# Optimization experiments

Hardware: AMD Instinct MI355X
Metric: run time of the kernel (lower is better)

Reference implementation:

```python
import jax, jax.numpy as jnp
import numpy as np

N_NODES = 50000
N_EDGES = 200000
NODE_DIM = 160     # node feat dim (divisible by 5 per wrapper slicing)
EDGE_DIM = 64      # latent edge feat dim
RAW_EDGE_DIM = 8   # raw geometric edge attributes
HID = 256          # hidden dim of edge/node update MLPs
ENC_HID = 128      # hidden dim of EASP edge encoder
N_ITER = 3
ENC_IN = 2 * NODE_DIM + RAW_EDGE_DIM                 # 328
EDGE_IN = 2 * 2 * NODE_DIM + 2 * EDGE_DIM            # 768 (reattach -> factor 2)
MSG_IN = 2 * NODE_DIM + EDGE_DIM                     # 384 (reattach node + edge)


def _ln(x, g, b):
    mu = jnp.mean(x, axis=-1, keepdims=True)
    v = jnp.var(x, axis=-1, keepdims=True)
    return (x - mu) * jax.lax.rsqrt(v + 1e-5) * g + b


def setup_inputs() -> dict:
    key = jax.random.key(0)
    ks = jax.random.split(key, 24)

    def w(k, shape):
        return (jax.random.normal(k, shape, jnp.float32) / np.sqrt(shape[0])).astype(jnp.float32)

    return {
        'x': jax.random.normal(ks[0], (N_NODES, NODE_DIM), jnp.float32),
        'edge_attr': jax.random.normal(ks[1], (N_EDGES, RAW_EDGE_DIM), jnp.float32),
        # EASP edge encoder MLP
        'enc_W1': w(ks[2], (ENC_IN, ENC_HID)), 'enc_b1': jnp.zeros((ENC_HID,), jnp.float32),
        'enc_W2': w(ks[3], (ENC_HID, EDGE_DIM)), 'enc_b2': jnp.zeros((EDGE_DIM,), jnp.float32),
        # EdgeCNN edge update MLP
        'eW1': w(ks[4], (EDGE_IN, HID)), 'eb1': jnp.zeros((HID,), jnp.float32),
        'eW2': w(ks[5], (HID, EDGE_DIM)), 'eb2': jnp.zeros((EDGE_DIM,), jnp.float32),
        # AttentionNodeUpdateNet: per-edge message MLP + attention vector + node out
        'mW1': w(ks[6], (MSG_IN, HID)), 'mb1': jnp.zeros((HID,), jnp.float32),
        'att_v': w(ks[7], (HID,)),
        'nW1': w(ks[8], (HID, NODE_DIM)), 'nb1': jnp.zeros((NODE_DIM,), jnp.float32),
        # shared LayerNorms (ModuleList([layer]*n_iter) shares one layer)
        'ln_ng': jnp.ones((NODE_DIM,), jnp.float32), 'ln_nb': jnp.zeros((NODE_DIM,), jnp.float32),
        'ln_eg': jnp.ones((EDGE_DIM,), jnp.float32), 'ln_eb': jnp.zeros((EDGE_DIM,), jnp.float32),
        'edge_row': jax.random.randint(ks[9], (N_EDGES,), 0, N_NODES, jnp.int32),
        'edge_col': jax.random.randint(ks[10], (N_EDGES,), 0, N_NODES, jnp.int32),
    }


def reference(x, edge_attr, enc_W1, enc_b1, enc_W2, enc_b2, eW1, eb1, eW2, eb2,
              mW1, mb1, att_v, nW1, nb1, ln_ng, ln_nb, ln_eg, ln_eb,
              edge_row, edge_col):
    row, col = edge_row, edge_col
    # edge encoder: gather endpoints, encode raw edge attrs
    init_edge = jnp.concatenate([x[row], x[col], edge_attr], axis=1)  # [E, 328]
    init_edge = jnp.maximum(init_edge @ enc_W1 + enc_b1, 0.0) @ enc_W2 + enc_b2  # [E, 64]

    node_lat, edge_lat = x, init_edge
    for _ in range(N_ITER):
        nl = jnp.concatenate([x, node_lat], axis=1)            # reattach initial node feats [N, 320]
        el = jnp.concatenate([init_edge, edge_lat], axis=1)    # reattach initial edge feats [E, 128]
        # edge update: gather-concat-MLP
        e_in = jnp.concatenate([nl[row], nl[col], el], axis=1)  # [E, 768]
        new_edge = jnp.maximum(e_in @ eW1 + eb1, 0.0) @ eW2 + eb2  # [E, 64]
        # node update: per-edge message + segment-softmax attention + scatter agg
        msg = jnp.maximum(jnp.concatenate([nl[col], new_edge], axis=1) @ mW1 + mb1, 0.0)  # [E, 256]
        logit = jax.nn.leaky_relu(msg @ att_v, 0.2)             # [E]
        smax = jax.ops.segment_max(logit, row, num_segments=N_NODES)
        ex = jnp.exp(logit - smax[row])
        den = jax.ops.segment_sum(ex, row, num_segments=N_NODES)
        alpha = ex / (den[row] + 1e-16)
        agg = jax.ops.segment_sum(alpha[:, None] * msg, row, num_segments=N_NODES)  # [N, 256]
        new_node = agg @ nW1 + nb1                              # [N, 160]
        # residual skip + (shared) LayerNorm
        node_lat = _ln(x + new_node, ln_ng, ln_nb)
        edge_lat = _ln(init_edge + new_edge, ln_eg, ln_eb)
    return node_lat, edge_lat
```

## Files before the change

### kernel.cpp

```cpp
#include <hip/hip_runtime.h>
#include <stdint.h>

#define N_NODES 50000
#define N_EDGES 200000
#define SCAN_B 512

typedef __bf16 bf16_t;
typedef bf16_t bf16x8 __attribute__((ext_vector_type(8)));
typedef float f32x4 __attribute__((ext_vector_type(4)));

__device__ __forceinline__ float bf2f(ushort h) {
  union { unsigned int u; float f; } c; c.u = ((unsigned int)h) << 16; return c.f;
}
__device__ __forceinline__ ushort f2bf(float f) {
  union { float f; unsigned int u; } c; c.f = f;
  unsigned int r = (c.u >> 16) & 1u;
  c.u += 0x7fffu + r;
  return (ushort)(c.u >> 16);
}
__device__ __forceinline__ float wave_sum(float v) {
#pragma unroll
  for (int m = 32; m > 0; m >>= 1) v += __shfl_xor(v, m, 64);
  return v;
}

__global__ void detect_k(const ushort* x, unsigned int* flag) {
  int i = blockIdx.x * 256 + threadIdx.x;
  unsigned int cnt = 0;
  for (int j = i; j < 1000000; j += 64 * 256) {
    ushort v = x[j];
    if (((v & 0x7F80u) == 0x7F80u) && (v & 0x7Fu)) cnt++;
  }
  if (cnt) atomicAdd(flag, cnt);
}

__global__ void cvt_in_k(const void* src, ushort* dst, int n, const unsigned int* flag) {
  int i = blockIdx.x * 256 + threadIdx.x;
  if (i >= n) return;
  if (*flag >= 2) dst[i] = f2bf(((const float*)src)[i]);
  else            dst[i] = ((const ushort*)src)[i];
}

__global__ void cvt_eattr_k(const void* src, const int* perm, ushort* dst,
                            const unsigned int* flag) {
  int i = blockIdx.x * 256 + threadIdx.x;
  if (i >= N_EDGES * 8) return;
  int e = i >> 3, j = i & 7;
  size_t o = (size_t)perm[e] * 8 + j;
  if (*flag >= 2) dst[i] = f2bf(((const float*)src)[o]);
  else            dst[i] = ((const ushort*)src)[o];
}

__global__ void transpose2_k(const void* W, ushort* Bt, int k0, int Ksrc, int Kpad,
                             int Wstride, const unsigned int* flag) {
  int k = blockIdx.x * 256 + threadIdx.x;
  int n = blockIdx.y;
  if (k >= Kpad) return;
  ushort v = 0;
  if (k < Ksrc) {
    if (*flag >= 2) v = f2bf(((const float*)W)[(size_t)(k0 + k) * Wstride + n]);
    else            v = ((const ushort*)W)[(size_t)(k0 + k) * Wstride + n];
  }
  Bt[(size_t)n * Kpad + k] = v;
}

__global__ void hist_k(const int* row, int* deg) {
  int e = blockIdx.x * 256 + threadIdx.x;
  if (e < N_EDGES) atomicAdd(&deg[row[e]], 1);
}
__global__ void scan_blk_k(const int* deg, int* off, int* bsum, int n) {
  __shared__ int s[SCAN_B];
  int i = blockIdx.x * SCAN_B + threadIdx.x;
  int v = (i < n) ? deg[i] : 0;
  s[threadIdx.x] = v;
  __syncthreads();
  for (int o = 1; o < SCAN_B; o <<= 1) {
    int t = (threadIdx.x >= o) ? s[threadIdx.x - o] : 0;
    __syncthreads();
    s[threadIdx.x] += t;
    __syncthreads();
  }
  if (i < n) off[i] = s[threadIdx.x] - v;
  if (threadIdx.x == SCAN_B - 1) bsum[blockIdx.x] = s[SCAN_B - 1];
}
__global__ void scan_top_k(int* bsum, int nb) {
  __shared__ int s[128];
  int v = (threadIdx.x < nb) ? bsum[threadIdx.x] : 0;
  s[threadIdx.x] = v;
  __syncthreads();
  for (int o = 1; o < 128; o <<= 1) {
    int t = (threadIdx.x >= o) ? s[threadIdx.x - o] : 0;
    __syncthreads();
    s[threadIdx.x] += t;
    __syncthreads();
  }
  if (threadIdx.x < nb) bsum[threadIdx.x] = s[threadIdx.x] - v;
}
__global__ void scan_add_k(int* off, const int* bsum, int n) {
  int i = blockIdx.x * 256 + threadIdx.x;
  if (i < n) off[i] += bsum[i >> 9];
  if (i == 0) off[n] = N_EDGES;
}
__global__ void fill_k(const int* row, const int* off, int* cur, int* perm) {
  int e = blockIdx.x * 256 + threadIdx.x;
  if (e >= N_EDGES) return;
  int r = row[e];
  int p = off[r] + atomicAdd(&cur[r], 1);
  perm[p] = e;
}
__global__ void gather_rc_k(const int* row, const int* col, const int* perm,
                            int* rs, int* cs) {
  int e = blockIdx.x * 256 + threadIdx.x;
  if (e >= N_EDGES) return;
  int o = perm[e];
  rs[e] = row[o];
  cs[e] = col[o];
}

struct GemmP {
  const ushort* X;
  const ushort* L;
  const ushort* E2;
  const float*  Af;
  const int* row;
  const int* col;
  const ushort* Bt;
  const ushort* bias;
  const ushort* Cr;
  const ushort* Cc;
  long cst;
  ushort* outb;  long ob_stride;
  ushort* outb2; long ob2_stride;
  float*  outf;  long of_stride;
  long e2s;
  int M, K, Nw;
};

template <int MODE>
__device__ __forceinline__ uint4 load_a8(const GemmP& p, int e, int kg) {
  if (MODE == 0) {
    return *(const uint4*)(p.E2 + (size_t)e * p.e2s + kg);
  } else if (MODE == 5) {
    if (kg < 160) return *(const uint4*)(p.X + (size_t)e * 160 + kg);
    return *(const uint4*)(p.L + (size_t)e * 160 + (kg - 160));
  } else if (MODE == 7) {
    if (kg < 160) return *(const uint4*)(p.X + (size_t)e * 160 + kg);
    uint4 z; z.x = z.y = z.z = z.w = 0u; return z;
  } else if (MODE == 8) {
    if (kg < 8) return *(const uint4*)(p.E2 + (size_t)e * 8);
    uint4 z; z.x = z.y = z.z = z.w = 0u; return z;
  } else {
    const float* s = p.Af + (size_t)e * p.K + kg;
    f32x4 f0 = *(const f32x4*)s;
    f32x4 f1 = *(const f32x4*)(s + 4);
    union { ushort r[8]; uint4 u; } o;
    o.r[0] = f2bf(f0[0]); o.r[1] = f2bf(f0[1]); o.r[2] = f2bf(f0[2]); o.r[3] = f2bf(f0[3]);
    o.r[4] = f2bf(f1[0]); o.r[5] = f2bf(f1[1]); o.r[6] = f2bf(f1[2]); o.r[7] = f2bf(f1[3]);
    return o.u;
  }
}

template <int MODE, int CI, bool RELU, int NT>
__global__ __launch_bounds__(256) void gemm_k(GemmP p) {
  constexpr int BR = NT / 2;
  constexpr int NTC = NT * 16;
  __shared__ __align__(16) ushort smem[9216 + 1152 * NT];
  ushort* Asm = smem;
  ushort* Bsm = smem + 9216;
  const int t = threadIdx.x;
  const int w = t >> 6;
  const int l = t & 63;
  const int m0 = blockIdx.x * 128;
  const int n0 = blockIdx.y * NTC;

  const int srow = t >> 1;
  const int sph = (t & 1) << 5;
  int e = m0 + srow;
  if (e >= p.M) e = p.M - 1;

  int bn_[BR], bk_[BR];
#pragma unroll
  for (int j = 0; j < BR; j++) {
    int cid = j * 256 + t;
    bn_[j] = cid >> 3;
    bk_[j] = (cid & 7) << 3;
  }

  const int mq = l & 15;
  const int qd = l >> 4;

  uint4 ar[4];
  uint4 br[BR];
  auto load_tile = [&](int k0) {
#pragma unroll
    for (int j = 0; j < 4; j++)
      ar[j] = load_a8<MODE>(p, e, k0 + sph + j * 8);
#pragma unroll
    for (int j = 0; j < BR; j++)
      br[j] = *(const uint4*)(p.Bt + (size_t)(n0 + bn_[j]) * p.K + k0 + bk_[j]);
  };

  load_tile(0);

  f32x4 acc[2][NT] = {};
  if (CI) {
#pragma unroll
    for (int mt = 0; mt < 2; mt++) {
#pragma unroll
      for (int i = 0; i < 4; i++) {
        int r = m0 + w * 32 + mt * 16 + qd * 4 + i;
        if (r >= p.M) r = p.M - 1;
        const ushort* pc = p.Cc + (size_t)p.col[r] * p.cst + n0 + mq;
        const ushort* pr = nullptr;
        if (CI == 1) pr = p.Cr + (size_t)p.row[r] * p.cst + n0 + mq;
#pragma unroll
        for (int nt = 0; nt < NT; nt++) {
          float v = bf2f(pc[nt * 16]);
          if (CI == 1) v += bf2f(pr[nt * 16]);
          acc[mt][nt][i] = v;
        }
      }
    }
  }

  const int kiters = p.K >> 6;
  for (int kt = 0; kt < kiters; kt++) {
    __syncthreads();
#pragma unroll
    for (int j = 0; j < 4; j++)
      *(uint4*)&Asm[srow * 72 + sph + j * 8] = ar[j];
#pragma unroll
    for (int j = 0; j < BR; j++)
      *(uint4*)&Bsm[bn_[j] * 72 + bk_[j]] = br[j];
    if (kt + 1 < kiters) load_tile((kt + 1) << 6);
    __syncthreads();
#pragma unroll
    for (int ph = 0; ph < 2; ph++) {
      uint4 ra0 = *(const uint4*)&Asm[(w * 32 + mq) * 72 + ph * 32 + qd * 8];
      uint4 ra1 = *(const uint4*)&Asm[(w * 32 + 16 + mq) * 72 + ph * 32 + qd * 8];
      bf16x8 af0 = __builtin_bit_cast(bf16x8, ra0);
      bf16x8 af1 = __builtin_bit_cast(bf16x8, ra1);
#pragma unroll
      for (int nt = 0; nt < NT; nt++) {
        uint4 rb = *(const uint4*)&Bsm[(nt * 16 + mq) * 72 + ph * 32 + qd * 8];
        bf16x8 bfv = __builtin_bit_cast(bf16x8, rb);
        acc[0][nt] = __builtin_amdgcn_mfma_f32_16x16x32_bf16(af0, bfv, acc[0][nt], 0, 0, 0);
        acc[1][nt] = __builtin_amdgcn_mfma_f32_16x16x32_bf16(af1, bfv, acc[1][nt], 0, 0, 0);
      }
    }
  }

  if (MODE == 4) {
#pragma unroll
    for (int mt = 0; mt < 2; mt++) {
#pragma unroll
      for (int nt = 0; nt < NT; nt++) {
        int c = n0 + nt * 16 + mq;
        float bv = bf2f(p.bias[c]);
#pragma unroll
        for (int i = 0; i < 4; i++) {
          int r = m0 + w * 32 + mt * 16 + qd * 4 + i;
          if (r >= p.M) continue;
          float v = acc[mt][nt][i] + bv;
          if (RELU) v = fmaxf(v, 0.0f);
          p.outf[(size_t)r * p.of_stride + c] = v;
        }
      }
    }
  } else {
    __syncthreads();
    ushort* S = smem + w * (32 * NTC);
#pragma unroll
    for (int mt = 0; mt < 2; mt++) {
#pragma unroll
      for (int nt = 0; nt < NT; nt++) {
        float bv = bf2f(p.bias[n0 + nt * 16 + mq]);
#pragma unroll
        for (int i = 0; i < 4; i++) {
          float v = acc[mt][nt][i] + bv;
          if (RELU) v = fmaxf(v, 0.0f);
          S[(mt * 16 + qd * 4 + i) * NTC + nt * 16 + mq] = f2bf(v);
        }
      }
    }
    __syncthreads();
#pragma unroll
    for (int j = 0; j < NT; j++) {
      int flat = (j * 64 + l) * 8;
      int lr = flat / NTC, cc = flat % NTC;
      int r = m0 + w * 32 + lr;
      if (r < p.M) {
        uint4 v = *(const uint4*)&S[lr * NTC + cc];
        *(uint4*)(p.outb + (size_t)r * p.ob_stride + n0 + cc) = v;
        if (p.outb2) *(uint4*)(p.outb2 + (size_t)r * p.ob2_stride + n0 + cc) = v;
      }
    }
  }
}

__global__ void copy_u4_k(const uint4* s, uint4* d, int n) {
  int i = blockIdx.x * 256 + threadIdx.x;
  if (i < n) d[i] = s[i];
}

__global__ void agg_csr_k(const ushort* msg, const ushort* att, const int* off,
                          float* agg) {
  int n = blockIdx.x * 4 + (threadIdx.x >> 6);
  int l = threadIdx.x & 63;
  if (n >= N_NODES) return;
  const int s0 = off[n], s1 = off[n + 1];
  ushort4 av = *(const ushort4*)(att + l * 4);
  const float a0 = bf2f(av.x), a1 = bf2f(av.y), a2 = bf2f(av.z), a3 = bf2f(av.w);
  float maxl = -1e30f;
  for (int j = s0; j < s1; j++) {
    ushort4 m = *(const ushort4*)(msg + (size_t)j * 256 + l * 4);
    float d = bf2f(m.x) * a0 + bf2f(m.y) * a1 + bf2f(m.z) * a2 + bf2f(m.w) * a3;
    d = wave_sum(d);
    float lg = (d > 0.0f) ? d : 0.2f * d;
    maxl = fmaxf(maxl, lg);
  }
  float den = 0.0f;
  f32x4 acc = {0.0f, 0.0f, 0.0f, 0.0f};
  for (int j = s0; j < s1; j++) {
    ushort4 m = *(const ushort4*)(msg + (size_t)j * 256 + l * 4);
    float m0 = bf2f(m.x), m1 = bf2f(m.y), m2 = bf2f(m.z), m3 = bf2f(m.w);
    float d = m0 * a0 + m1 * a1 + m2 * a2 + m3 * a3;
    d = wave_sum(d);
    float lg = (d > 0.0f) ? d : 0.2f * d;
    float ex = __expf(lg - maxl);
    den += ex;
    acc[0] += ex * m0; acc[1] += ex * m1; acc[2] += ex * m2; acc[3] += ex * m3;
  }
  float inv = 1.0f / (den + 1e-16f);
  f32x4 o = {acc[0] * inv, acc[1] * inv, acc[2] * inv, acc[3] * inv};
  *(f32x4*)(agg + (size_t)n * 256 + l * 4) = o;
}

__global__ void ln_node_k(const ushort* x, const float* nn, const ushort* g,
                          const ushort* b, ushort* nlat) {
  int n = blockIdx.x * 4 + (threadIdx.x >> 6);
  int l = threadIdx.x & 63;
  if (n >= N_NODES) return;
  size_t bx = (size_t)n * 160;
  float v0 = bf2f(x[bx + l]) + nn[bx + l];
  float v1 = bf2f(x[bx + 64 + l]) + nn[bx + 64 + l];
  float v2 = (l < 32) ? (bf2f(x[bx + 128 + l]) + nn[bx + 128 + l]) : 0.0f;
  float mu = wave_sum(v0 + v1 + v2) * (1.0f / 160.0f);
  float d0 = v0 - mu, d1 = v1 - mu;
  float d2 = (l < 32) ? (v2 - mu) : 0.0f;
  float var = wave_sum(d0 * d0 + d1 * d1 + d2 * d2) * (1.0f / 160.0f);
  float inv = rsqrtf(var + 1e-5f);
  nlat[bx + l]      = f2bf(d0 * inv * bf2f(g[l])      + bf2f(b[l]));
  nlat[bx + 64 + l] = f2bf(d1 * inv * bf2f(g[64 + l]) + bf2f(b[64 + l]));
  if (l < 32)
    nlat[bx + 128 + l] = f2bf(d2 * inv * bf2f(g[128 + l]) + bf2f(b[128 + l]));
}

__global__ void ln_edge_k(const ushort* g, const ushort* b, ushort* el) {
  int e = blockIdx.x * 4 + (threadIdx.x >> 6);
  int l = threadIdx.x & 63;
  if (e >= N_EDGES) return;
  float v = bf2f(el[(size_t)e * 128 + l]) + bf2f(el[(size_t)e * 128 + 64 + l]);
  float mu = wave_sum(v) * (1.0f / 64.0f);
  float d = v - mu;
  float var = wave_sum(d * d) * (1.0f / 64.0f);
  float inv = rsqrtf(var + 1e-5f);
  el[(size_t)e * 128 + 64 + l] = f2bf(d * inv * bf2f(g[l]) + bf2f(b[l]));
}

__global__ void out_node_k(const ushort* nlat, void* out, const unsigned int* flag) {
  int i = blockIdx.x * 256 + threadIdx.x;
  if (i >= N_NODES * 160) return;
  if (*flag >= 2) ((float*)out)[i] = bf2f(nlat[i]);
  else            ((ushort*)out)[i] = nlat[i];
}
__global__ void out_edge_k(const ushort* el, const int* perm, void* out,
                           const unsigned int* flag) {
  int i = blockIdx.x * 256 + threadIdx.x;
  if (i >= N_EDGES * 64) return;
  int e = i >> 6, c = i & 63;
  ushort v = el[(size_t)e * 128 + 64 + c];
  size_t o = (size_t)N_NODES * 160 + (size_t)perm[e] * 64 + c;
  if (*flag >= 2) ((float*)out)[o] = bf2f(v);
  else            ((ushort*)out)[o] = v;
}

extern "C" void kernel_launch(void* const* d_in, const int* in_sizes, int n_in,
                              void* d_out, int out_size, void* d_ws, size_t ws_size,
                              hipStream_t stream) {
  const void* x_r     = d_in[0];
  const void* eattr_r = d_in[1];
  const void* encW1   = d_in[2];
  const void* encb1_r = d_in[3];
  const void* encW2   = d_in[4];
  const void* encb2_r = d_in[5];
  const void* eW1     = d_in[6];
  const void* eb1_r   = d_in[7];
  const void* eW2     = d_in[8];
  const void* eb2_r   = d_in[9];
  const void* mW1     = d_in[10];
  const void* mb1_r   = d_in[11];
  const void* attv_r  = d_in[12];
  const void* nW1     = d_in[13];
  const void* nb1_r   = d_in[14];
  const void* lnng_r  = d_in[15];
  const void* lnnb_r  = d_in[16];
  const void* lneg_r  = d_in[17];
  const void* lneb_r  = d_in[18];
  const int* erow = (const int*)d_in[19];
  const int* ecol = (const int*)d_in[20];
  (void)in_sizes; (void)n_in;

  char* ws = (char*)d_ws;
  size_t off = 0;
  auto alloc = [&](size_t bytes) -> void* {
    void* p = ws + off;
    off = (off + bytes + 511) & ~(size_t)511;
    return p;
  };
  ushort* hm   = (ushort*)alloc((size_t)N_EDGES * 256 * 2);
  ushort* el   = (ushort*)alloc((size_t)N_EDGES * 128 * 2);
  float*  agg  = (float*)alloc((size_t)N_NODES * 256 * 4);
  ushort* xc   = (ushort*)alloc((size_t)N_NODES * 160 * 2);
  ushort* nlat = (ushort*)alloc((size_t)N_NODES * 160 * 2);
  ushort* Qc   = (ushort*)alloc((size_t)N_NODES * 256 * 2);
  int* degcur  = (int*)alloc((size_t)2 * N_NODES * 4);
  int* offcsr  = (int*)alloc((size_t)(N_NODES + 1) * 4);
  int* perm    = (int*)alloc((size_t)N_EDGES * 4);
  int* rs      = (int*)alloc((size_t)N_EDGES * 4);
  int* cs      = (int*)alloc((size_t)N_EDGES * 4);
  int* bsum    = (int*)alloc((size_t)128 * 4);
  ushort* BtPe = (ushort*)alloc((size_t)256 * 192 * 2);
  ushort* BtWenc = (ushort*)alloc((size_t)128 * 64 * 2);
  ushort* BtE2 = (ushort*)alloc((size_t)64 * 128 * 2);
  ushort* BtP  = (ushort*)alloc((size_t)512 * 320 * 2);
  ushort* BtWe = (ushort*)alloc((size_t)256 * 128 * 2);
  ushort* Bte2 = (ushort*)alloc((size_t)64 * 256 * 2);
  ushort* BtQ  = (ushort*)alloc((size_t)256 * 320 * 2);
  ushort* BtWm = (ushort*)alloc((size_t)256 * 64 * 2);
  ushort* Btn1 = (ushort*)alloc((size_t)160 * 256 * 2);
  ushort* pool = (ushort*)alloc((size_t)4096 * 2);
  unsigned int* flag = (unsigned int*)alloc(64);
  ushort* msg = hm;
  float*  nnf = (float*)hm;
  ushort* eac  = (ushort*)agg;
  ushort* Penc = (ushort*)((char*)agg + (size_t)N_EDGES * 8 * 2);
  ushort* Prc  = (ushort*)agg;
  ushort* zb   = pool + 2048;

  ushort* encb1c = pool;        ushort* encb2c = pool + 128;
  ushort* eb1c   = pool + 192;  ushort* eb2c   = pool + 448;
  ushort* mb1c   = pool + 512;  ushort* attvc  = pool + 768;
  ushort* nb1c   = pool + 1024; ushort* lnngc  = pool + 1184;
  ushort* lnnbc  = pool + 1344; ushort* lnegc  = pool + 1504;
  ushort* lnebc  = pool + 1568;

  if (off > ws_size) {
    hipMemsetAsync(d_out, 0, (size_t)out_size * 2, stream);
    return;
  }

  hipMemsetAsync(flag, 0, 64, stream);
  hipMemsetAsync(pool, 0, 4096 * 2, stream);
  hipMemsetAsync(degcur, 0, (size_t)2 * N_NODES * 4, stream);

  detect_k<<<64, 256, 0, stream>>>((const ushort*)x_r, flag);

  {
    int* deg = degcur;
    int* cur = degcur + N_NODES;
    const int nb = (N_NODES + SCAN_B - 1) / SCAN_B;
    hist_k<<<(N_EDGES + 255) / 256, 256, 0, stream>>>(erow, deg);
    scan_blk_k<<<nb, SCAN_B, 0, stream>>>(deg, offcsr, bsum, N_NODES);
    scan_top_k<<<1, 128, 0, stream>>>(bsum, nb);
    scan_add_k<<<(N_NODES + 255) / 256, 256, 0, stream>>>(offcsr, bsum, N_NODES);
    fill_k<<<(N_EDGES + 255) / 256, 256, 0, stream>>>(erow, offcsr, cur, perm);
    gather_rc_k<<<(N_EDGES + 255) / 256, 256, 0, stream>>>(erow, ecol, perm, rs, cs);
  }

  cvt_in_k<<<(N_NODES * 160 + 255) / 256, 256, 0, stream>>>(x_r, xc, N_NODES * 160, flag);
  cvt_eattr_k<<<(N_EDGES * 8 + 255) / 256, 256, 0, stream>>>(eattr_r, perm, eac, flag);
  cvt_in_k<<<1, 256, 0, stream>>>(encb1_r, encb1c, 128, flag);
  cvt_in_k<<<1, 256, 0, stream>>>(encb2_r, encb2c, 64, flag);
  cvt_in_k<<<1, 256, 0, stream>>>(eb1_r, eb1c, 256, flag);
  cvt_in_k<<<1, 256, 0, stream>>>(eb2_r, eb2c, 64, flag);
  cvt_in_k<<<1, 256, 0, stream>>>(mb1_r, mb1c, 256, flag);
  cvt_in_k<<<1, 256, 0, stream>>>(attv_r, attvc, 256, flag);
  cvt_in_k<<<1, 256, 0, stream>>>(nb1_r, nb1c, 160, flag);
  cvt_in_k<<<1, 256, 0, stream>>>(lnng_r, lnngc, 160, flag);
  cvt_in_k<<<1, 256, 0, stream>>>(lnnb_r, lnnbc, 160, flag);
  cvt_in_k<<<1, 256, 0, stream>>>(lneg_r, lnegc, 64, flag);
  cvt_in_k<<<1, 256, 0, stream>>>(lneb_r, lnebc, 64, flag);

  transpose2_k<<<dim3(1, 128), 256, 0, stream>>>(encW1, BtPe,             0, 160, 192, 128, flag);
  transpose2_k<<<dim3(1, 128), 256, 0, stream>>>(encW1, BtPe + 128 * 192, 160, 160, 192, 128, flag);
  transpose2_k<<<dim3(1, 128), 256, 0, stream>>>(encW1, BtWenc,           320, 8, 64, 128, flag);
  transpose2_k<<<dim3(1, 64), 256, 0, stream>>>(encW2, BtE2, 0, 128, 128, 64, flag);
  transpose2_k<<<dim3(2, 256), 256, 0, stream>>>(eW1, BtP,             0, 320, 320, 256, flag);
  transpose2_k<<<dim3(2, 256), 256, 0, stream>>>(eW1, BtP + 256 * 320, 320, 320, 320, 256, flag);
  transpose2_k<<<dim3(1, 256), 256, 0, stream>>>(eW1, BtWe, 640, 128, 128, 256, flag);
  transpose2_k<<<dim3(1, 64), 256, 0, stream>>>(eW2, Bte2, 0, 256, 256, 64, flag);
  transpose2_k<<<dim3(2, 256), 256, 0, stream>>>(mW1, BtQ, 0, 320, 320, 256, flag);
  transpose2_k<<<dim3(1, 256), 256, 0, stream>>>(mW1, BtWm, 320, 64, 64, 256, flag);
  transpose2_k<<<dim3(1, 160), 256, 0, stream>>>(nW1, Btn1, 0, 256, 256, 160, flag);

  copy_u4_k<<<(N_NODES * 160 / 8 + 255) / 256, 256, 0, stream>>>(
      (const uint4*)xc, (uint4*)nlat, N_NODES * 160 / 8);

  const int gE = (N_EDGES + 127) / 128;
  const int gN = (N_NODES + 127) / 128;

  {
    GemmP p{};
    p.X = xc; p.Bt = BtPe; p.bias = zb;
    p.outb = Penc; p.ob_stride = 256;
    p.M = N_NODES; p.K = 192; p.Nw = 256;
    gemm_k<7, 0, false, 8><<<dim3(gN, 2), 256, 0, stream>>>(p);
  }
  {
    GemmP p{};
    p.E2 = eac; p.row = rs; p.col = cs;
    p.Cr = Penc; p.Cc = Penc + 128; p.cst = 256;
    p.Bt = BtWenc; p.bias = encb1c;
    p.outb = hm; p.ob_stride = 128;
    p.M = N_EDGES; p.K = 64; p.Nw = 128;
    gemm_k<8, 1, true, 8><<<dim3(gE, 1), 256, 0, stream>>>(p);
  }
  {
    GemmP p{};
    p.E2 = hm; p.e2s = 128; p.Bt = BtE2; p.bias = encb2c;
    p.outb = el; p.ob_stride = 128;
    p.outb2 = el + 64; p.ob2_stride = 128;
    p.M = N_EDGES; p.K = 128; p.Nw = 64;
    gemm_k<0, 0, false, 4><<<dim3(gE, 1), 256, 0, stream>>>(p);
  }

  for (int it = 0; it < 3; it++) {
    {
      GemmP p{};
      p.X = xc; p.L = nlat; p.Bt = BtP; p.bias = zb;
      p.outb = Prc; p.ob_stride = 512;
      p.M = N_NODES; p.K = 320; p.Nw = 512;
      gemm_k<5, 0, false, 8><<<dim3(gN, 4), 256, 0, stream>>>(p);
    }
    {
      GemmP p{};
      p.X = xc; p.L = nlat; p.Bt = BtQ; p.bias = zb;
      p.outb = Qc; p.ob_stride = 256;
      p.M = N_NODES; p.K = 320; p.Nw = 256;
      gemm_k<5, 0, false, 8><<<dim3(gN, 2), 256, 0, stream>>>(p);
    }
    {
      GemmP p{};
      p.E2 = el; p.e2s = 128; p.row = rs; p.col = cs;
      p.Cr = Prc; p.Cc = Prc + 256; p.cst = 512;
      p.Bt = BtWe; p.bias = eb1c;
      p.outb = hm; p.ob_stride = 256;
      p.M = N_EDGES; p.K = 128; p.Nw = 256;
      gemm_k<0, 1, true, 8><<<dim3(gE, 2), 256, 0, stream>>>(p);
    }
    {
      GemmP p{};
      p.E2 = hm; p.e2s = 256; p.Bt = Bte2; p.bias = eb2c;
      p.outb = el + 64; p.ob_stride = 128;
      p.M = N_EDGES; p.K = 256; p.Nw = 64;
      gemm_k<0, 0, false, 4><<<dim3(gE, 1), 256, 0, stream>>>(p);
    }
    {
      GemmP p{};
      p.E2 = el + 64; p.e2s = 128; p.row = rs; p.col = cs;
      p.Cc = Qc; p.cst = 256;
      p.Bt = BtWm; p.bias = mb1c;
      p.outb = msg; p.ob_stride = 256;
      p.M = N_EDGES; p.K = 64; p.Nw = 256;
      gemm_k<0, 2, true, 8><<<dim3(gE, 2), 256, 0, stream>>>(p);
    }
    ln_edge_k<<<N_EDGES / 4, 256, 0, stream>>>(lnegc, lnebc, el);
    agg_csr_k<<<(N_NODES + 3) / 4, 256, 0, stream>>>(msg, attvc, offcsr, agg);
    {
      GemmP p{};
      p.Af = agg; p.Bt = Btn1; p.bias = nb1c;
      p.outf = nnf; p.of_stride = 160;
      p.M = N_NODES; p.K = 256; p.Nw = 160;
      gemm_k<4, 0, false, 10><<<dim3(gN, 1), 256, 0, stream>>>(p);
    }
    ln_node_k<<<(N_NODES + 3) / 4, 256, 0, stream>>>(xc, nnf, lnngc, lnnbc, nlat);
  }

  out_node_k<<<(N_NODES * 160 + 255) / 256, 256, 0, stream>>>(nlat, d_out, flag);
  out_edge_k<<<(N_EDGES * 64 + 255) / 256, 256, 0, stream>>>(el, perm, d_out, flag);
  (void)out_size;
}
```

Baseline: 1.814 ms.

## Stage gathered node projections through LDS and merge P/Q node GEMMs

```diff
diff --git a/kernel.cpp b/kernel.cpp
--- a/kernel.cpp
+++ b/kernel.cpp
@@ -131,6 +131,8 @@
   long cst;
   ushort* outb;  long ob_stride;
   ushort* outb2; long ob2_stride;
+  ushort* outS;  long oS_stride;
+  int nsplit;
   float*  outf;  long of_stride;
   long e2s;
   int M, K, Nw;
@@ -164,6 +166,7 @@
 __global__ __launch_bounds__(256) void gemm_k(GemmP p) {
   constexpr int BR = NT / 2;
   constexpr int NTC = NT * 16;
+  constexpr int CIP = NTC + 8;
   __shared__ __align__(16) ushort smem[9216 + 1152 * NT];
   ushort* Asm = smem;
   ushort* Bsm = smem + 9216;
@@ -204,22 +207,26 @@
 
   f32x4 acc[2][NT] = {};
   if (CI) {
-#pragma unroll
-    for (int mt = 0; mt < 2; mt++) {
-#pragma unroll
-      for (int i = 0; i < 4; i++) {
-        int r = m0 + w * 32 + mt * 16 + qd * 4 + i;
-        if (r >= p.M) r = p.M - 1;
-        const ushort* pc = p.Cc + (size_t)p.col[r] * p.cst + n0 + mq;
-        const ushort* pr = nullptr;
-        if (CI == 1) pr = p.Cr + (size_t)p.row[r] * p.cst + n0 + mq;
-#pragma unroll
-        for (int nt = 0; nt < NT; nt++) {
-          float v = bf2f(pc[nt * 16]);
-          if (CI == 1) v += bf2f(pr[nt * 16]);
-          acc[mt][nt][i] = v;
+    const int gph = (t & 1) * (NTC / 2);
+#pragma unroll
+    for (int rd = 0; rd < ((CI == 1) ? 2 : 1); rd++) {
+      int node = (rd == 0) ? p.col[e] : p.row[e];
+      const ushort* base = ((rd == 0) ? p.Cc : p.Cr) + (size_t)node * p.cst + n0 + gph;
+#pragma unroll
+      for (int j = 0; j < NTC / 16; j++)
+        *(uint4*)&smem[srow * CIP + gph + j * 8] = *(const uint4*)(base + j * 8);
+      __syncthreads();
+#pragma unroll
+      for (int mt = 0; mt < 2; mt++) {
+#pragma unroll
+        for (int i = 0; i < 4; i++) {
+          int rl = w * 32 + mt * 16 + qd * 4 + i;
+#pragma unroll
+          for (int nt = 0; nt < NT; nt++)
+            acc[mt][nt][i] += bf2f(smem[rl * CIP + nt * 16 + mq]);
         }
       }
+      __syncthreads();
     }
   }
 
@@ -268,8 +275,12 @@
       }
     }
   } else {
-    __syncthreads();
-    ushort* S = smem + w * (32 * NTC);
+    ushort* dst = p.outb;
+    long dstr = p.ob_stride;
+    int nb0 = n0;
+    if (p.outS && n0 >= p.nsplit) { dst = p.outS; dstr = p.oS_stride; nb0 = n0 - p.nsplit; }
+    __syncthreads();
+    ushort* S = smem + w * (32 * CIP);
 #pragma unroll
     for (int mt = 0; mt < 2; mt++) {
 #pragma unroll
@@ -279,7 +290,7 @@
         for (int i = 0; i < 4; i++) {
           float v = acc[mt][nt][i] + bv;
           if (RELU) v = fmaxf(v, 0.0f);
-          S[(mt * 16 + qd * 4 + i) * NTC + nt * 16 + mq] = f2bf(v);
+          S[(mt * 16 + qd * 4 + i) * CIP + nt * 16 + mq] = f2bf(v);
         }
       }
     }
@@ -290,8 +301,8 @@
       int lr = flat / NTC, cc = flat % NTC;
       int r = m0 + w * 32 + lr;
       if (r < p.M) {
-        uint4 v = *(const uint4*)&S[lr * NTC + cc];
-        *(uint4*)(p.outb + (size_t)r * p.ob_stride + n0 + cc) = v;
+        uint4 v = *(const uint4*)&S[lr * CIP + cc];
+        *(uint4*)(dst + (size_t)r * dstr + nb0 + cc) = v;
         if (p.outb2) *(uint4*)(p.outb2 + (size_t)r * p.ob2_stride + n0 + cc) = v;
       }
     }
@@ -433,10 +444,9 @@
   ushort* BtPe = (ushort*)alloc((size_t)256 * 192 * 2);
   ushort* BtWenc = (ushort*)alloc((size_t)128 * 64 * 2);
   ushort* BtE2 = (ushort*)alloc((size_t)64 * 128 * 2);
-  ushort* BtP  = (ushort*)alloc((size_t)512 * 320 * 2);
+  ushort* BtPQ = (ushort*)alloc((size_t)768 * 320 * 2);
   ushort* BtWe = (ushort*)alloc((size_t)256 * 128 * 2);
   ushort* Bte2 = (ushort*)alloc((size_t)64 * 256 * 2);
-  ushort* BtQ  = (ushort*)alloc((size_t)256 * 320 * 2);
   ushort* BtWm = (ushort*)alloc((size_t)256 * 64 * 2);
   ushort* Btn1 = (ushort*)alloc((size_t)160 * 256 * 2);
   ushort* pool = (ushort*)alloc((size_t)4096 * 2);
@@ -496,11 +506,11 @@
   transpose2_k<<<dim3(1, 128), 256, 0, stream>>>(encW1, BtPe + 128 * 192, 160, 160, 192, 128, flag);
   transpose2_k<<<dim3(1, 128), 256, 0, stream>>>(encW1, BtWenc,           320, 8, 64, 128, flag);
   transpose2_k<<<dim3(1, 64), 256, 0, stream>>>(encW2, BtE2, 0, 128, 128, 64, flag);
-  transpose2_k<<<dim3(2, 256), 256, 0, stream>>>(eW1, BtP,             0, 320, 320, 256, flag);
-  transpose2_k<<<dim3(2, 256), 256, 0, stream>>>(eW1, BtP + 256 * 320, 320, 320, 320, 256, flag);
+  transpose2_k<<<dim3(2, 256), 256, 0, stream>>>(eW1, BtPQ,             0, 320, 320, 256, flag);
+  transpose2_k<<<dim3(2, 256), 256, 0, stream>>>(eW1, BtPQ + 256 * 320, 320, 320, 320, 256, flag);
+  transpose2_k<<<dim3(2, 256), 256, 0, stream>>>(mW1, BtPQ + 512 * 320, 0, 320, 320, 256, flag);
   transpose2_k<<<dim3(1, 256), 256, 0, stream>>>(eW1, BtWe, 640, 128, 128, 256, flag);
   transpose2_k<<<dim3(1, 64), 256, 0, stream>>>(eW2, Bte2, 0, 256, 256, 64, flag);
-  transpose2_k<<<dim3(2, 256), 256, 0, stream>>>(mW1, BtQ, 0, 320, 320, 256, flag);
   transpose2_k<<<dim3(1, 256), 256, 0, stream>>>(mW1, BtWm, 320, 64, 64, 256, flag);
   transpose2_k<<<dim3(1, 160), 256, 0, stream>>>(nW1, Btn1, 0, 256, 256, 160, flag);
 
@@ -538,17 +548,11 @@
   for (int it = 0; it < 3; it++) {
     {
       GemmP p{};
-      p.X = xc; p.L = nlat; p.Bt = BtP; p.bias = zb;
+      p.X = xc; p.L = nlat; p.Bt = BtPQ; p.bias = zb;
       p.outb = Prc; p.ob_stride = 512;
-      p.M = N_NODES; p.K = 320; p.Nw = 512;
-      gemm_k<5, 0, false, 8><<<dim3(gN, 4), 256, 0, stream>>>(p);
-    }
-    {
-      GemmP p{};
-      p.X = xc; p.L = nlat; p.Bt = BtQ; p.bias = zb;
-      p.outb = Qc; p.ob_stride = 256;
-      p.M = N_NODES; p.K = 320; p.Nw = 256;
-      gemm_k<5, 0, false, 8><<<dim3(gN, 2), 256, 0, stream>>>(p);
+      p.outS = Qc; p.oS_stride = 256; p.nsplit = 512;
+      p.M = N_NODES; p.K = 320; p.Nw = 768;
+      gemm_k<5, 0, false, 8><<<dim3(gN, 6), 256, 0, stream>>>(p);
     }
     {
       GemmP p{};
```

Result: slower. 1.875 ms (+3.3%).
